# Kernel tuning notes

Hardware: AMD Instinct MI355X
Metric: run time of the kernel (lower is better)

Reference implementation:

```python
import jax, jax.numpy as jnp
import numpy as np

D_MODEL = 768
N_HEAD = 12
D_HEAD = 64


def setup_inputs() -> dict:
    key = jax.random.key(0)
    k1, k2, k3, k4, k5 = jax.random.split(key, 5)
    B, T = 8, 1024
    hidden_states = jax.random.normal(k1, (B, T, D_MODEL), dtype=jnp.float32)
    # torch Linear weights are [out, in]; we store [in, out] and use x @ W
    scale_attn = 1.0 / np.sqrt(D_MODEL)
    W_attn = jax.random.normal(k2, (D_MODEL, 3 * D_MODEL), dtype=jnp.float32) * scale_attn
    b_attn = jax.random.normal(k3, (3 * D_MODEL,), dtype=jnp.float32) * 0.02
    W_proj = jax.random.normal(k4, (D_MODEL, D_MODEL), dtype=jnp.float32) * scale_attn
    b_proj = jax.random.normal(k5, (D_MODEL,), dtype=jnp.float32) * 0.02
    return {"hidden_states": hidden_states, "W_attn": W_attn, "b_attn": b_attn,
            "W_proj": W_proj, "b_proj": b_proj}


def reference(hidden_states, W_attn, b_attn, W_proj, b_proj):
    B, T, _ = hidden_states.shape
    qkv = hidden_states @ W_attn + b_attn                     # [B, T, 3*D]
    Q, K, V = jnp.split(qkv, 3, axis=-1)
    def heads(x):  # [B, T, D] -> [B, H, T, d]
        return x.reshape(B, T, N_HEAD, D_HEAD).transpose(0, 2, 1, 3)
    Q, K, V = heads(Q), heads(K), heads(V)
    # past_key_values=None -> T_full == T, q_start == 0: standard causal mask
    scores = jnp.einsum('bhqd,bhkd->bhqk', Q, K) / np.sqrt(D_HEAD)
    causal = jnp.tril(jnp.ones((T, T), dtype=bool))
    scores = jnp.where(causal, scores, -jnp.inf)
    attn = jax.nn.softmax(scores, axis=-1)
    values = jnp.einsum('bhqk,bhkd->bhqd', attn, V)          # dropout = identity (eval)
    values = values.transpose(0, 2, 1, 3).reshape(B, T, D_MODEL)
    out = values @ W_proj + b_proj
    return out, K, V
```

## Files before the change

kernel.cpp:

```cpp
#include <hip/hip_runtime.h>
#include <stdint.h>

#define B_SZ 8
#define T_SZ 1024
#define DM   768
#define NH   12
#define DH   64
#define NTOK (B_SZ * T_SZ)
#define NOUT (NTOK * DM)
#define INF  __builtin_inff()

typedef unsigned short u16;
typedef __attribute__((ext_vector_type(8))) short short8;
typedef __attribute__((ext_vector_type(4))) short short4v;
typedef __attribute__((ext_vector_type(4))) float f32x4;

#define MFMA16x16x32 __builtin_amdgcn_mfma_f32_16x16x32_bf16

__device__ __forceinline__ u16 f2bf(float f) {
    unsigned u = __builtin_bit_cast(unsigned, f);
    u += 0x7fffu + ((u >> 16) & 1u);
    return (u16)(u >> 16);
}

__device__ __forceinline__ f32x4 max4(f32x4 a, f32x4 b) {
    f32x4 r; r.x = fmaxf(a.x, b.x); r.y = fmaxf(a.y, b.y);
    r.z = fmaxf(a.z, b.z); r.w = fmaxf(a.w, b.w); return r;
}
__device__ __forceinline__ f32x4 add4(f32x4 a, f32x4 b) {
    f32x4 r; r.x = a.x + b.x; r.y = a.y + b.y;
    r.z = a.z + b.z; r.w = a.w + b.w; return r;
}

__device__ __forceinline__ void gload16(const void* g, void* l) {
    __builtin_amdgcn_global_load_lds(
        (const __attribute__((address_space(1))) unsigned int*)(unsigned long long)(uintptr_t)g,
        (__attribute__((address_space(3))) unsigned int*)(unsigned int)(uintptr_t)l,
        16, 0, 0);
}

__global__ __launch_bounds__(256) void cvt_bf16_kernel(const float* __restrict__ in,
                                                       u16* __restrict__ out, int n) {
    int i = (blockIdx.x * 256 + threadIdx.x) * 4;
    if (i >= n) return;
    f32x4 v = *(const f32x4*)(in + i);
    short4v o;
    o.x = (short)f2bf(v.x); o.y = (short)f2bf(v.y);
    o.z = (short)f2bf(v.z); o.w = (short)f2bf(v.w);
    *(short4v*)(out + i) = o;
}

__global__ __launch_bounds__(256) void transpose_bf16_kernel(const float* __restrict__ in,
                                                             u16* __restrict__ out,
                                                             int R, int C) {
    __shared__ float tile[32][33];
    int tx = threadIdx.x & 31, ty = threadIdx.x >> 5;
    int c0 = blockIdx.x * 32, r0 = blockIdx.y * 32;
    for (int i = ty; i < 32; i += 8)
        tile[i][tx] = in[(size_t)(r0 + i) * C + c0 + tx];
    __syncthreads();
    for (int i = ty; i < 32; i += 8)
        out[(size_t)(c0 + i) * R + r0 + tx] = f2bf(tile[tx][i]);
}

__global__ __launch_bounds__(256) void transpose_v_kernel(const float* __restrict__ in,
                                                          u16* __restrict__ out) {
    __shared__ float tile[32][33];
    const int head = blockIdx.z;
    const int t0 = blockIdx.x * 32, d0 = blockIdx.y * 32;
    const float* ip = in + (size_t)head * 65536;
    u16* op = out + (size_t)head * 65536;
    int tx = threadIdx.x & 31, ty = threadIdx.x >> 5;
    for (int i = ty; i < 32; i += 8)
        tile[i][tx] = ip[(size_t)(t0 + i) * 64 + d0 + tx];
    __syncthreads();
    for (int i = ty; i < 32; i += 8)
        op[(size_t)(d0 + i) * 1024 + t0 + tx] = f2bf(tile[tx][i]);
}

template <int EPI>
__global__ __launch_bounds__(256, 3) void gemm_k768_kernel(
    const u16* __restrict__ A, const u16* __restrict__ BT, const float* __restrict__ bias,
    u16* __restrict__ qbf, u16* __restrict__ kbf,
    float* __restrict__ outK, float* __restrict__ outV, float* __restrict__ outP)
{
    __shared__ alignas(16) u16 As[3][128 * 32];
    __shared__ alignas(16) u16 Bs[3][128 * 32];
    const int t   = threadIdx.x;
    const int wid = t >> 6, l = t & 63;
    const int lr  = l & 15, g = l >> 4;
    const int m0  = blockIdx.x * 128, n0 = blockIdx.y * 128;
    const int wm  = (wid >> 1) * 64, wn = (wid & 1) * 64;

    const int srow = t >> 2;
    const int sch  = ((t & 3) ^ ((srow >> 1) & 3)) * 8;
    const u16* ga0 = A  + (size_t)(m0 + srow) * 768 + sch;
    const u16* ga1 = A  + (size_t)(m0 + 64 + srow) * 768 + sch;
    const u16* gb0 = BT + (size_t)(n0 + srow) * 768 + sch;
    const u16* gb1 = BT + (size_t)(n0 + 64 + srow) * 768 + sch;

#define GSTAGE(buf, kt) do {                              \
        gload16(ga0 + (kt) * 32, As[buf] + t * 8);        \
        gload16(ga1 + (kt) * 32, As[buf] + 2048 + t * 8); \
        gload16(gb0 + (kt) * 32, Bs[buf] + t * 8);        \
        gload16(gb1 + (kt) * 32, Bs[buf] + 2048 + t * 8); \
    } while (0)

    const int fco = (g ^ ((lr >> 1) & 3)) * 8;

    f32x4 acc[4][4] = {};

#define COMPUTE(buf) do {                                                 \
        const u16* aB = As[buf];                                          \
        const u16* bB = Bs[buf];                                          \
        short8 af[4], bfr[4];                                             \
        _Pragma("unroll")                                                 \
        for (int i = 0; i < 4; ++i)                                       \
            af[i] = *(const short8*)(aB + (wm + i * 16 + lr) * 32 + fco); \
        _Pragma("unroll")                                                 \
        for (int j = 0; j < 4; ++j)                                       \
            bfr[j] = *(const short8*)(bB + (wn + j * 16 + lr) * 32 + fco);\
        __builtin_amdgcn_s_setprio(1);                                    \
        _Pragma("unroll")                                                 \
        for (int i = 0; i < 4; ++i)                                       \
            _Pragma("unroll")                                             \
            for (int j = 0; j < 4; ++j)                                   \
                acc[i][j] = MFMA16x16x32(af[i], bfr[j], acc[i][j], 0, 0, 0);\
        __builtin_amdgcn_s_setprio(0);                                    \
    } while (0)

#define WAITBAR(N) do {                                           \
        asm volatile("s_waitcnt vmcnt(" #N ")" ::: "memory");     \
        __builtin_amdgcn_s_barrier();                             \
        __builtin_amdgcn_sched_barrier(0);                        \
    } while (0)

    GSTAGE(0, 0); GSTAGE(1, 1);
    WAITBAR(4);

    #pragma unroll 1
    for (int i = 0; i < 7; ++i) {
        const int kt = i * 3;
        GSTAGE(2, kt + 2); COMPUTE(0); WAITBAR(4);
        GSTAGE(0, kt + 3); COMPUTE(1); WAITBAR(4);
        GSTAGE(1, kt + 4); COMPUTE(2); WAITBAR(4);
    }
    GSTAGE(2, 23); COMPUTE(0); WAITBAR(4);
    COMPUTE(1); WAITBAR(0);
    COMPUTE(2);
#undef GSTAGE
#undef COMPUTE
#undef WAITBAR

    #pragma unroll
    for (int j = 0; j < 4; ++j) {
        const int n = n0 + wn + j * 16 + lr;
        const float bn = bias[n];
        if (EPI == 0) {
            const int which = n / 768;
            const int hd = n - which * 768;
            const int h = hd >> 6, dd = hd & 63;
            #pragma unroll
            for (int i = 0; i < 4; ++i) {
                #pragma unroll
                for (int r = 0; r < 4; ++r) {
                    const int m = m0 + wm + i * 16 + g * 4 + r;
                    const int b = m >> 10, tt = m & 1023;
                    const int idx = ((b * 12 + h) * 1024 + tt) * 64 + dd;
                    const float v = acc[i][j][r] + bn;
                    if (which == 0) {
                        qbf[idx] = f2bf(v * (0.125f * 1.44269504f));
                    } else if (which == 1) {
                        outK[idx] = v; kbf[idx] = f2bf(v);
                    } else {
                        outV[idx] = v;
                    }
                }
            }
        } else {
            #pragma unroll
            for (int i = 0; i < 4; ++i)
                #pragma unroll
                for (int r = 0; r < 4; ++r) {
                    const int m = m0 + wm + i * 16 + g * 4 + r;
                    outP[(size_t)m * 768 + n] = acc[i][j][r] + bn;
                }
        }
    }
}

__global__ __launch_bounds__(256, 3) void attn_kernel(
    const u16* __restrict__ Qb, const u16* __restrict__ Kb,
    const u16* __restrict__ Vt, u16* __restrict__ Ob)
{
    __shared__ alignas(16) u16 Ks[2][4096];
    __shared__ alignas(16) u16 Vs[2][4096];
    __shared__ alignas(16) u16 Pl[4][16 * 72];
    const int bh = blockIdx.x;
    const int t = threadIdx.x;
    const int wid = t >> 6, l = t & 63;
    const int c = l & 15, g = l >> 4;
    u16* P = Pl[wid];
    const u16* Kp = Kb + (size_t)bh * 65536;
    const u16* Vp = Vt + (size_t)bh * 65536;
    const int b = bh / 12, h = bh - (bh / 12) * 12;

    const int srow = t >> 3;
    const int sch  = (t & 7) ^ (srow & 7);
    const u16* Ksrc0 = Kp + (size_t)srow * 64 + sch * 8;
    const u16* Ksrc1 = Kp + (size_t)(srow + 32) * 64 + sch * 8;
    const u16* Vsrc0 = Vp + (size_t)srow * 1024 + sch * 8;
    const u16* Vsrc1 = Vp + (size_t)(srow + 32) * 1024 + sch * 8;

    const int fo0 = c * 64 + ((g ^ (c & 7)) * 8);
    const int fo1 = c * 64 + (((g + 4) ^ (c & 7)) * 8);

#define STAGE(buf, kt0) do {                                        \
        gload16(Ksrc0 + (size_t)(kt0) * 64, Ks[buf] + t * 8);       \
        gload16(Ksrc1 + (size_t)(kt0) * 64, Ks[buf] + 2048 + t * 8);\
        gload16(Vsrc0 + (kt0),              Vs[buf] + t * 8);       \
        gload16(Vsrc1 + (kt0),              Vs[buf] + 2048 + t * 8);\
    } while (0)

    #pragma unroll 1
    for (int pass = 0; pass < 2; ++pass) {
        const int tile = pass ? (15 - blockIdx.y) : blockIdx.y;
        const int qbase = tile * 64 + wid * 16;
        const int qg = qbase + c;
        const u16* Qp = Qb + ((size_t)bh * 1024 + qg) * 64 + g * 8;
        const short8 bq0 = *(const short8*)(Qp);
        const short8 bq1 = *(const short8*)(Qp + 32);

        f32x4 oacc[4] = {};
        float mrow = -INF, lpart = 0.f;
        const int nb = tile + 1;

        STAGE(0, 0);
        __syncthreads();
        int cur = 0;

        #pragma unroll 1
        for (int kb = 0; kb < nb; ++kb) {
            if (kb + 1 < nb) STAGE(cur ^ 1, (kb + 1) << 6);
            const u16* kB = Ks[cur];
            const u16* vB = Vs[cur];
            short8 af0[4], af1[4], vf0[4], vf1[4];
            #pragma unroll
            for (int j = 0; j < 4; ++j) {
                af0[j] = *(const short8*)(kB + j * 1024 + fo0);
                af1[j] = *(const short8*)(kB + j * 1024 + fo1);
            }
            #pragma unroll
            for (int dt = 0; dt < 4; ++dt) {
                vf0[dt] = *(const short8*)(vB + dt * 1024 + fo0);
                vf1[dt] = *(const short8*)(vB + dt * 1024 + fo1);
            }
            f32x4 s[4] = {};
            __builtin_amdgcn_s_setprio(1);
            #pragma unroll
            for (int j = 0; j < 4; ++j) {
                s[j] = MFMA16x16x32(af0[j], bq0, s[j], 0, 0, 0);
                s[j] = MFMA16x16x32(af1[j], bq1, s[j], 0, 0, 0);
            }
            __builtin_amdgcn_s_setprio(0);
            if (kb == nb - 1) {
                const int kt0 = kb << 6;
                #pragma unroll
                for (int j = 0; j < 4; ++j)
                    #pragma unroll
                    for (int r = 0; r < 4; ++r)
                        if (kt0 + j * 16 + g * 4 + r > qg) s[j][r] = -INF;
            }
            f32x4 mm = max4(max4(s[0], s[1]), max4(s[2], s[3]));
            float tm = fmaxf(fmaxf(mm.x, mm.y), fmaxf(mm.z, mm.w));
            tm = fmaxf(tm, __shfl_xor(tm, 16));
            tm = fmaxf(tm, __shfl_xor(tm, 32));
            const bool keep = (__all(tm <= mrow + 8.f) != 0);
            const float mnew = keep ? mrow : fmaxf(mrow, tm);
            if (!keep) {
                const float sc = exp2f(mrow - mnew);
                mrow = mnew;
                lpart *= sc;
                #pragma unroll
                for (int dt = 0; dt < 4; ++dt) {
                    oacc[dt][0] *= sc; oacc[dt][1] *= sc;
                    oacc[dt][2] *= sc; oacc[dt][3] *= sc;
                }
            }
            f32x4 p[4];
            #pragma unroll
            for (int j = 0; j < 4; ++j) {
                p[j].x = exp2f(s[j].x - mnew); p[j].y = exp2f(s[j].y - mnew);
                p[j].z = exp2f(s[j].z - mnew); p[j].w = exp2f(s[j].w - mnew);
            }
            f32x4 ps = add4(add4(p[0], p[1]), add4(p[2], p[3]));
            lpart += (ps.x + ps.y) + (ps.z + ps.w);
            #pragma unroll
            for (int j = 0; j < 4; ++j) {
                short4v w;
                w.x = (short)f2bf(p[j].x); w.y = (short)f2bf(p[j].y);
                w.z = (short)f2bf(p[j].z); w.w = (short)f2bf(p[j].w);
                *(short4v*)(P + c * 72 + j * 16 + g * 4) = w;
            }
            const short8 pf0 = *(const short8*)(P + c * 72 + g * 8);
            const short8 pf1 = *(const short8*)(P + c * 72 + 32 + g * 8);
            __builtin_amdgcn_s_setprio(1);
            #pragma unroll
            for (int dt = 0; dt < 4; ++dt) {
                oacc[dt] = MFMA16x16x32(vf0[dt], pf0, oacc[dt], 0, 0, 0);
                oacc[dt] = MFMA16x16x32(vf1[dt], pf1, oacc[dt], 0, 0, 0);
            }
            __builtin_amdgcn_s_setprio(0);
            __syncthreads();
            cur ^= 1;
        }
        float lsum = lpart;
        lsum += __shfl_xor(lsum, 16);
        lsum += __shfl_xor(lsum, 32);
        const float li = 1.f / lsum;
        #pragma unroll
        for (int dt = 0; dt < 4; ++dt) {
            short4v o;
            o.x = (short)f2bf(oacc[dt][0] * li);
            o.y = (short)f2bf(oacc[dt][1] * li);
            o.z = (short)f2bf(oacc[dt][2] * li);
            o.w = (short)f2bf(oacc[dt][3] * li);
            *(short4v*)(Ob + (size_t)(b * 1024 + qg) * 768 + h * 64 + dt * 16 + g * 4) = o;
        }
    }
#undef STAGE
}

extern "C" void kernel_launch(void* const* d_in, const int* in_sizes, int n_in,
                              void* d_out, int out_size, void* d_ws, size_t ws_size,
                              hipStream_t stream) {
    const float* hs = (const float*)d_in[0];
    const float* Wa = (const float*)d_in[1];
    const float* ba = (const float*)d_in[2];
    const float* Wp = (const float*)d_in[3];
    const float* bp = (const float*)d_in[4];
    float* out = (float*)d_out;

    u16* ws  = (u16*)d_ws;
    u16* Xbf = ws;
    u16* WaT = Xbf + NOUT;
    u16* WpT = WaT + 768 * 2304;
    u16* Qbf = WpT + 768 * 768;
    u16* Kbf = Qbf + NOUT;
    u16* VTb = Kbf + NOUT;
    u16* Obf = VTb + NOUT;

    cvt_bf16_kernel<<<NOUT / 1024, 256, 0, stream>>>(hs, Xbf, NOUT);
    transpose_bf16_kernel<<<dim3(2304 / 32, 768 / 32), 256, 0, stream>>>(Wa, WaT, 768, 2304);
    transpose_bf16_kernel<<<dim3(768 / 32, 768 / 32), 256, 0, stream>>>(Wp, WpT, 768, 768);
    gemm_k768_kernel<0><<<dim3(64, 18), 256, 0, stream>>>(
        Xbf, WaT, ba, Qbf, Kbf, out + NOUT, out + 2 * (size_t)NOUT, nullptr);
    transpose_v_kernel<<<dim3(32, 2, 96), 256, 0, stream>>>(out + 2 * (size_t)NOUT, VTb);
    attn_kernel<<<dim3(96, 8), 256, 0, stream>>>(Qbf, Kbf, VTb, Obf);
    gemm_k768_kernel<1><<<dim3(64, 6), 256, 0, stream>>>(
        Obf, WpT, bp, nullptr, nullptr, nullptr, nullptr, out);
}
```

Baseline: 126.7 us.

## Merge prep kernels into one launch and load V fragments directly from global

The bf16 conversion of hidden states and the two weight transposes are merged into a single prep_kernel launch, dispatched by block index, to remove two kernel launches. In the attention kernel, V tiles are no longer staged through LDS with async global-to-LDS loads. Each lane instead reads its V^T fragments straight from global memory at the top of each key block, which halves LDS usage and may raise occupancy. The risk is exposed global-load latency on V that the LDS double buffer used to hide, plus less coalesced access.

Measured after the change: 143.2 us. 13.0% more time.

```diff
diff --git a/kernel.cpp b/kernel.cpp
--- a/kernel.cpp
+++ b/kernel.cpp
@@ -39,23 +39,32 @@
         16, 0, 0);
 }
 
-__global__ __launch_bounds__(256) void cvt_bf16_kernel(const float* __restrict__ in,
-                                                       u16* __restrict__ out, int n) {
-    int i = (blockIdx.x * 256 + threadIdx.x) * 4;
-    if (i >= n) return;
-    f32x4 v = *(const f32x4*)(in + i);
-    short4v o;
-    o.x = (short)f2bf(v.x); o.y = (short)f2bf(v.y);
-    o.z = (short)f2bf(v.z); o.w = (short)f2bf(v.w);
-    *(short4v*)(out + i) = o;
-}
-
-__global__ __launch_bounds__(256) void transpose_bf16_kernel(const float* __restrict__ in,
-                                                             u16* __restrict__ out,
-                                                             int R, int C) {
+__global__ __launch_bounds__(256) void prep_kernel(
+    const float* __restrict__ hs, u16* __restrict__ Xbf,
+    const float* __restrict__ Wa, u16* __restrict__ WaT,
+    const float* __restrict__ Wp, u16* __restrict__ WpT)
+{
     __shared__ float tile[32][33];
-    int tx = threadIdx.x & 31, ty = threadIdx.x >> 5;
-    int c0 = blockIdx.x * 32, r0 = blockIdx.y * 32;
+    const int bid = blockIdx.x;
+    if (bid < 6144) {
+        const int i = bid * 1024 + threadIdx.x * 4;
+        f32x4 v = *(const f32x4*)(hs + i);
+        short4v o;
+        o.x = (short)f2bf(v.x); o.y = (short)f2bf(v.y);
+        o.z = (short)f2bf(v.z); o.w = (short)f2bf(v.w);
+        *(short4v*)(Xbf + i) = o;
+        return;
+    }
+    const float* in; u16* out; int R, C, bx, by;
+    if (bid < 6144 + 1728) {
+        const int lid = bid - 6144;
+        in = Wa; out = WaT; R = 768; C = 2304; bx = lid % 72; by = lid / 72;
+    } else {
+        const int lid = bid - 7872;
+        in = Wp; out = WpT; R = 768; C = 768; bx = lid % 24; by = lid / 24;
+    }
+    const int tx = threadIdx.x & 31, ty = threadIdx.x >> 5;
+    const int c0 = bx * 32, r0 = by * 32;
     for (int i = ty; i < 32; i += 8)
         tile[i][tx] = in[(size_t)(r0 + i) * C + c0 + tx];
     __syncthreads();
@@ -194,7 +203,6 @@
     const u16* __restrict__ Vt, u16* __restrict__ Ob)
 {
     __shared__ alignas(16) u16 Ks[2][4096];
-    __shared__ alignas(16) u16 Vs[2][4096];
     __shared__ alignas(16) u16 Pl[4][16 * 72];
     const int bh = blockIdx.x;
     const int t = threadIdx.x;
@@ -209,8 +217,6 @@
     const int sch  = (t & 7) ^ (srow & 7);
     const u16* Ksrc0 = Kp + (size_t)srow * 64 + sch * 8;
     const u16* Ksrc1 = Kp + (size_t)(srow + 32) * 64 + sch * 8;
-    const u16* Vsrc0 = Vp + (size_t)srow * 1024 + sch * 8;
-    const u16* Vsrc1 = Vp + (size_t)(srow + 32) * 1024 + sch * 8;
 
     const int fo0 = c * 64 + ((g ^ (c & 7)) * 8);
     const int fo1 = c * 64 + (((g + 4) ^ (c & 7)) * 8);
@@ -218,8 +224,6 @@
 #define STAGE(buf, kt0) do {                                        \
         gload16(Ksrc0 + (size_t)(kt0) * 64, Ks[buf] + t * 8);       \
         gload16(Ksrc1 + (size_t)(kt0) * 64, Ks[buf] + 2048 + t * 8);\
-        gload16(Vsrc0 + (kt0),              Vs[buf] + t * 8);       \
-        gload16(Vsrc1 + (kt0),              Vs[buf] + 2048 + t * 8);\
     } while (0)
 
     #pragma unroll 1
@@ -241,20 +245,22 @@
 
         #pragma unroll 1
         for (int kb = 0; kb < nb; ++kb) {
-            if (kb + 1 < nb) STAGE(cur ^ 1, (kb + 1) << 6);
+            const int kt0 = kb << 6;
+            short8 vf0[4], vf1[4];
+            #pragma unroll
+            for (int dt = 0; dt < 4; ++dt) {
+                const u16* vrow = Vp + (size_t)(dt * 16 + c) * 1024 + kt0 + g * 8;
+                vf0[dt] = *(const short8*)(vrow);
+                vf1[dt] = *(const short8*)(vrow + 32);
+            }
+            if (kb + 1 < nb) STAGE(cur ^ 1, kt0 + 64);
             const u16* kB = Ks[cur];
-            const u16* vB = Vs[cur];
-            short8 af0[4], af1[4], vf0[4], vf1[4];
+            short8 af0[4], af1[4];
             #pragma unroll
             for (int j = 0; j < 4; ++j) {
                 af0[j] = *(const short8*)(kB + j * 1024 + fo0);
                 af1[j] = *(const short8*)(kB + j * 1024 + fo1);
             }
-            #pragma unroll
-            for (int dt = 0; dt < 4; ++dt) {
-                vf0[dt] = *(const short8*)(vB + dt * 1024 + fo0);
-                vf1[dt] = *(const short8*)(vB + dt * 1024 + fo1);
-            }
             f32x4 s[4] = {};
             __builtin_amdgcn_s_setprio(1);
             #pragma unroll
@@ -264,7 +270,6 @@
             }
             __builtin_amdgcn_s_setprio(0);
             if (kb == nb - 1) {
-                const int kt0 = kb << 6;
                 #pragma unroll
                 for (int j = 0; j < 4; ++j)
                     #pragma unroll
@@ -350,9 +355,7 @@
     u16* VTb = Kbf + NOUT;
     u16* Obf = VTb + NOUT;
 
-    cvt_bf16_kernel<<<NOUT / 1024, 256, 0, stream>>>(hs, Xbf, NOUT);
-    transpose_bf16_kernel<<<dim3(2304 / 32, 768 / 32), 256, 0, stream>>>(Wa, WaT, 768, 2304);
-    transpose_bf16_kernel<<<dim3(768 / 32, 768 / 32), 256, 0, stream>>>(Wp, WpT, 768, 768);
+    prep_kernel<<<8448, 256, 0, stream>>>(hs, Xbf, Wa, WaT, Wp, WpT);
     gemm_k768_kernel<0><<<dim3(64, 18), 256, 0, stream>>>(
         Xbf, WaT, ba, Qbf, Kbf, out + NOUT, out + 2 * (size_t)NOUT, nullptr);
     transpose_v_kernel<<<dim3(32, 2, 96), 256, 0, stream>>>(out + 2 * (size_t)NOUT, VTb);
```
